# Performance work log

Hardware: AMD Instinct MI355X
Metric: run time of the kernel (lower is better)

Reference implementation:

```python
import jax, jax.numpy as jnp
import numpy as np

B, NT, NC, NN = 2, 64, 1024, 1024
C, H = 1024, 16
HD = C // H
N = NT + NC + NN
EPS = 1e-5
NEG = -1e30


def _ln(t, w, b):
    # LayerNorm over last dim (head_dim), torch eps=1e-5
    mu = jnp.mean(t, axis=-1, keepdims=True)
    var = jnp.mean(jnp.square(t - mu), axis=-1, keepdims=True)
    return (t - mu) * jax.lax.rsqrt(var + EPS) * w + b


def _rope(q, k, pos):
    # q,k: [B,H,S,HD]; pos: [B,S]; rotate-half RoPE, base 10000
    hd = q.shape[-1]
    half = hd // 2
    inv_freq = 1.0 / (10000.0 ** (jnp.arange(half, dtype=jnp.float32) / half))
    ang = pos.astype(jnp.float32)[:, None, :, None] * inv_freq  # [B,1,S,half]
    cos, sin = jnp.cos(ang), jnp.sin(ang)
    def rot(t):
        t1, t2 = t[..., :half], t[..., half:]
        return jnp.concatenate([t1 * cos - t2 * sin, t2 * cos + t1 * sin], axis=-1)
    return rot(q), rot(k)


def setup_inputs() -> dict:
    key = jax.random.key(0)
    ks = jax.random.split(key, 4)
    s = 0.02
    return {
        "x": jax.random.normal(ks[0], (B, N, C), jnp.float32),
        "position_ids": jnp.broadcast_to(jnp.arange(NC + NN, dtype=jnp.int32), (B, NC + NN)),
        "text_position_ids": jnp.broadcast_to(jnp.arange(NT, dtype=jnp.int32), (B, NT)),
        "attention_mask": jnp.tril(jnp.ones((N, N), dtype=bool)),
        "n_text": NT, "n_clean": NC, "n_noised": NN,
        "qkv_w": jax.random.normal(ks[1], (3, 3 * C, C), jnp.float32) * s,
        "qkv_b": jnp.zeros((3, 3 * C), jnp.float32),
        "qn_w": jnp.ones((3, HD), jnp.float32),
        "qn_b": jnp.zeros((3, HD), jnp.float32),
        "kn_w": jnp.ones((3, HD), jnp.float32),
        "kn_b": jnp.zeros((3, HD), jnp.float32),
        "proj_w": jax.random.normal(ks[2], (3, C, C), jnp.float32) * s,
        "proj_b": jnp.zeros((3, C), jnp.float32),
    }


def reference(x, position_ids, text_position_ids, attention_mask, n_text, n_clean, n_noised,
              qkv_w, qkv_b, qn_w, qn_b, kn_w, kn_b, proj_w, proj_b):
    Bx, Nx, Cx = x.shape
    hd = qn_w.shape[-1]
    nh = Cx // hd
    b0, b1 = n_text, n_text + n_clean
    segs = (x[:, :b0], x[:, b0:b1], x[:, b1:])  # text / clean / noised

    qs, kks, vvs = [], [], []
    for i, xs in enumerate(segs):
        S = xs.shape[1]
        qkv = jnp.einsum('bsc,oc->bso', xs, qkv_w[i]) + qkv_b[i]
        qkv = qkv.reshape(Bx, S, 3, nh, hd).transpose(2, 0, 3, 1, 4)  # [3,B,H,S,hd]
        q = _ln(qkv[0], qn_w[i], qn_b[i])
        k = _ln(qkv[1], kn_w[i], kn_b[i])
        qs.append(q); kks.append(k); vvs.append(qkv[2])

    img_q = jnp.concatenate([qs[1], qs[2]], axis=2)
    img_k = jnp.concatenate([kks[1], kks[2]], axis=2)
    img_q, img_k = _rope(img_q, img_k, position_ids)
    txt_q, txt_k = _rope(qs[0], kks[0], text_position_ids)

    q = jnp.concatenate([txt_q, img_q], axis=2)
    k = jnp.concatenate([txt_k, img_k], axis=2)
    v = jnp.concatenate(vvs, axis=2)

    scale = 1.0 / np.sqrt(hd).astype(np.float32)
    scores = jnp.einsum('bhqd,bhkd->bhqk', q, k) * scale
    scores = jnp.where(attention_mask, scores, NEG)
    attn = jax.nn.softmax(scores, axis=-1)
    out = jnp.einsum('bhqk,bhkd->bhqd', attn, v)
    out = out.transpose(0, 2, 1, 3).reshape(Bx, Nx, Cx)

    o_segs = (out[:, :b0], out[:, b0:b1], out[:, b1:])
    outs = [jnp.einsum('bsc,oc->bso', o_segs[i], proj_w[i]) + proj_b[i] for i in range(3)]
    return jnp.concatenate(outs, axis=1)
```

## Files before the change

kernel.cpp:

```cpp
#include <hip/hip_runtime.h>
#include <hip/hip_bf16.h>

#define BB   2
#define NT   64
#define NC   1024
#define NN   1024
#define NTOK (NT + NC + NN)
#define CC   1024
#define HH   16
#define HD   64
#define K3   (3 * CC)
#define EPSV 1e-5f

typedef __attribute__((ext_vector_type(8))) short short8;
typedef __attribute__((ext_vector_type(4))) float f32x4;
typedef __attribute__((ext_vector_type(4))) float float4v;

__device__ __forceinline__ short bf16raw(float x) {
    __hip_bfloat16 h = __float2bfloat16(x);
    return *(short*)&h;
}

#define GL_LDS(gptr, lptr) \
    __builtin_amdgcn_global_load_lds( \
        (const __attribute__((address_space(1))) void*)(gptr), \
        (__attribute__((address_space(3))) void*)(lptr), 16, 0, 0)

__global__ __launch_bounds__(256) void cast_all(
    const float* __restrict__ s0, const float* __restrict__ s1, const float* __restrict__ s2,
    __hip_bfloat16* __restrict__ d0, __hip_bfloat16* __restrict__ d1, __hip_bfloat16* __restrict__ d2,
    int n0, int n1, int n2)
{
    int i = blockIdx.x * 256 + threadIdx.x;
    int stride = gridDim.x * 256;
    int ntot = n0 + n1 + n2;
    for (; i < ntot; i += stride) {
        const float* sp; short* dp; int j;
        if (i < n0)            { sp = s0; dp = (short*)d0; j = i; }
        else if (i < n0 + n1)  { sp = s1; dp = (short*)d1; j = i - n0; }
        else                   { sp = s2; dp = (short*)d2; j = i - n0 - n1; }
        float4v v = *(const float4v*)(sp + (size_t)j * 4);
        short4 o;
        o.x = bf16raw(v.x); o.y = bf16raw(v.y); o.z = bf16raw(v.z); o.w = bf16raw(v.w);
        *(short4*)(dp + (size_t)j * 4) = o;
    }
}

__global__ __launch_bounds__(256) void gemm_qkv(
    const __hip_bfloat16* __restrict__ A,
    const __hip_bfloat16* __restrict__ Wb,
    const float* __restrict__ biasb,
    const int* __restrict__ pos_ids,
    const int* __restrict__ tpos_ids,
    const float* __restrict__ qn_w, const float* __restrict__ qn_b,
    const float* __restrict__ kn_w, const float* __restrict__ kn_b,
    __hip_bfloat16* __restrict__ Q,
    __hip_bfloat16* __restrict__ Kg,
    __hip_bfloat16* __restrict__ Vt)
{
    __shared__ short buf[128 * 134];
    short* As = buf;
    short* Bs = buf + 8192;

    int tid = threadIdx.x;
    int lane = tid & 63, w = tid >> 6;
    int l15 = lane & 15, quad = lane >> 4;
    int wm = w >> 1, wn = w & 1;
    int r7 = l15 & 7;

    int y = blockIdx.y;
    int seg, tm;
    if (y < 16)      { seg = 1; tm = y * 128; }
    else if (y < 32) { seg = 2; tm = (y - 16) * 128; }
    else             { seg = 0; tm = 0; }
    int S = (seg == 0) ? 64 : 1024;
    int seg_start = (seg == 0) ? 0 : (seg == 1 ? NT : NT + NC);
    const short* W = (const short*)Wb + (size_t)seg * K3 * CC;
    const float* bias = biasb + (size_t)seg * K3;
    int tileN = blockIdx.x * 128;

    const short* aptr[4];
    const short* bptr[4];
#pragma unroll
    for (int j = 0; j < 4; ++j) {
        int c = j * 256 + tid;
        int row = c >> 3, u = (c & 7) ^ (row & 7);
        int ar = tm + row;
        int arow = (ar / S) * NTOK + seg_start + (ar % S);
        aptr[j] = (const short*)A + (size_t)arow * CC + u * 8;
        bptr[j] = W + (size_t)(tileN + row) * CC + u * 8;
    }

    f32x4 zero = {0.f, 0.f, 0.f, 0.f};
    f32x4 acc[4][4];
#pragma unroll
    for (int mb = 0; mb < 4; ++mb)
#pragma unroll
        for (int nb = 0; nb < 4; ++nb) acc[mb][nb] = zero;

    for (int k0 = 0; k0 < CC; k0 += 64) {
        __syncthreads();
#pragma unroll
        for (int j = 0; j < 4; ++j) {
            int c8 = (j * 256 + tid) * 8;
            GL_LDS(aptr[j] + k0, As + c8);
            GL_LDS(bptr[j] + k0, Bs + c8);
        }
        __syncthreads();

#pragma unroll
        for (int s = 0; s < 2; ++s) {
            int sx = ((s * 4 + quad) ^ r7) * 8;
            short8 af[4], bf[4];
#pragma unroll
            for (int mb = 0; mb < 4; ++mb)
                af[mb] = *(const short8*)&As[(wm * 64 + mb * 16 + l15) * 64 + sx];
#pragma unroll
            for (int nb = 0; nb < 4; ++nb)
                bf[nb] = *(const short8*)&Bs[(wn * 64 + nb * 16 + l15) * 64 + sx];
#pragma unroll
            for (int mb = 0; mb < 4; ++mb)
#pragma unroll
                for (int nb = 0; nb < 4; ++nb)
                    acc[mb][nb] = __builtin_amdgcn_mfma_f32_16x16x32_bf16(af[mb], bf[nb], acc[mb][nb], 0, 0, 0);
        }
    }

    int sect = tileN >> 10;
    __syncthreads();

    if (sect < 2) {
        const float* nw = (sect == 0 ? qn_w : kn_w) + seg * HD;
        const float* nbv = (sect == 0 ? qn_b : kn_b) + seg * HD;
        float lw[4], lb[4], bcol[4];
#pragma unroll
        for (int nb = 0; nb < 4; ++nb) {
            lw[nb] = nw[nb * 16 + l15];
            lb[nb] = nbv[nb * 16 + l15];
            bcol[nb] = bias[tileN + wn * 64 + nb * 16 + l15];
        }
        float invf0 = expf(-9.210340371976184f * (float)l15 * (1.0f / 32.0f));
        float invf1 = expf(-9.210340371976184f * (float)(16 + l15) * (1.0f / 32.0f));
        float qscale = (sect == 0) ? 0.125f : 1.0f;

#pragma unroll
        for (int mb = 0; mb < 4; ++mb) {
#pragma unroll
            for (int r = 0; r < 4; ++r) {
                int tok = wm * 64 + mb * 16 + quad * 4 + r;
                int ar = tm + tok;
                int bb = ar / S;
                int nloc = seg_start + (ar % S);
                float v[4];
#pragma unroll
                for (int nb = 0; nb < 4; ++nb) v[nb] = acc[mb][nb][r] + bcol[nb];

                float mu = v[0] + v[1] + v[2] + v[3];
#pragma unroll
                for (int off = 8; off >= 1; off >>= 1) mu += __shfl_xor(mu, off);
                mu *= (1.0f / 64.0f);
                float t[4];
                float var = 0.f;
#pragma unroll
                for (int nb = 0; nb < 4; ++nb) { t[nb] = v[nb] - mu; var += t[nb] * t[nb]; }
#pragma unroll
                for (int off = 8; off >= 1; off >>= 1) var += __shfl_xor(var, off);
                var *= (1.0f / 64.0f);
                float rstd = rsqrtf(var + EPSV);
#pragma unroll
                for (int nb = 0; nb < 4; ++nb) v[nb] = t[nb] * rstd * lw[nb] + lb[nb];

                int pos = (seg == 0) ? tpos_ids[bb * NT + nloc]
                                     : pos_ids[bb * (NC + NN) + (nloc - NT)];
                float s0, c0, s1, c1;
                sincosf((float)pos * invf0, &s0, &c0);
                sincosf((float)pos * invf1, &s1, &c1);
                short* bp = &buf[tok * 134 + wn * 64];
                bp[0 * 16 + l15] = bf16raw((v[0] * c0 - v[2] * s0) * qscale);
                bp[1 * 16 + l15] = bf16raw((v[1] * c1 - v[3] * s1) * qscale);
                bp[2 * 16 + l15] = bf16raw((v[2] * c0 + v[0] * s0) * qscale);
                bp[3 * 16 + l15] = bf16raw((v[3] * c1 + v[1] * s1) * qscale);
            }
        }
        __syncthreads();
        __hip_bfloat16* dst = (sect == 0) ? Q : Kg;
        int head_base = (tileN & 1023) >> 6;
#pragma unroll
        for (int it = 0; it < 8; ++it) {
            int idx = it * 256 + tid;
            int tok = idx >> 4, cc = (idx & 15) * 8;
            int ar = tm + tok;
            int bb = ar / S;
            int nloc = seg_start + (ar % S);
            int hh2 = head_base + (cc >> 6), d = cc & 63;
            *(short8*)((short*)dst + ((size_t)(bb * HH + hh2) * NTOK + nloc) * HD + d) =
                *(const short8*)&buf[tok * 134 + cc];
        }
    } else {
        float bcol[4];
#pragma unroll
        for (int nb = 0; nb < 4; ++nb) bcol[nb] = bias[tileN + wn * 64 + nb * 16 + l15];
#pragma unroll
        for (int mb = 0; mb < 4; ++mb) {
#pragma unroll
            for (int r = 0; r < 4; ++r) {
                int tok = wm * 64 + mb * 16 + quad * 4 + r;
#pragma unroll
                for (int nb = 0; nb < 4; ++nb) {
                    int col = wn * 64 + nb * 16 + l15;
                    buf[col * 134 + tok] = bf16raw(acc[mb][nb][r] + bcol[nb]);
                }
            }
        }
        __syncthreads();
#pragma unroll
        for (int it = 0; it < 8; ++it) {
            int idx = it * 256 + tid;
            int row = idx >> 4;
            int tc = (idx & 15) * 8;
            int vcol = (tileN - 2048) + row;
            int h = vcol >> 6, d = vcol & 63;
            int ar = tm + tc;
            int bb = ar / S;
            int nloc = seg_start + (ar % S);
            short8 val = *(const short8*)&buf[row * 134 + tc];
            *(short8*)((short*)Vt + ((size_t)(bb * HH + h) * HD + d) * NTOK + nloc) = val;
        }
    }
}

__global__ __launch_bounds__(256) void gemm_proj(
    const __hip_bfloat16* __restrict__ A,
    const __hip_bfloat16* __restrict__ Wb,
    const float* __restrict__ biasb,
    float* __restrict__ Cout)
{
    __shared__ short As[64 * 64];
    __shared__ short Bs[128 * 64];

    int tid = threadIdx.x;
    int lane = tid & 63, w = tid >> 6;
    int l15 = lane & 15, quad = lane >> 4;
    int wm = w >> 1, wn = w & 1;
    int r7 = l15 & 7;

    int y = blockIdx.y;
    int seg, tm;
    if (y < 32)      { seg = 1; tm = y * 64; }
    else if (y < 64) { seg = 2; tm = (y - 32) * 64; }
    else             { seg = 0; tm = (y - 64) * 64; }
    int S = (seg == 0) ? 64 : 1024;
    int seg_start = (seg == 0) ? 0 : (seg == 1 ? NT : NT + NC);
    const short* W = (const short*)Wb + (size_t)seg * CC * CC;
    const float* bias = biasb + (size_t)seg * CC;
    int tileN = blockIdx.x * 128;

    const short* aptr[2];
    const short* bptr[4];
#pragma unroll
    for (int j = 0; j < 2; ++j) {
        int c = j * 256 + tid;
        int row = c >> 3, u = (c & 7) ^ (row & 7);
        int ar = tm + row;
        int arow = (ar / S) * NTOK + seg_start + (ar % S);
        aptr[j] = (const short*)A + (size_t)arow * CC + u * 8;
    }
#pragma unroll
    for (int j = 0; j < 4; ++j) {
        int c = j * 256 + tid;
        int row = c >> 3, u = (c & 7) ^ (row & 7);
        bptr[j] = W + (size_t)(tileN + row) * CC + u * 8;
    }

    f32x4 zero = {0.f, 0.f, 0.f, 0.f};
    f32x4 acc[2][4];
#pragma unroll
    for (int mb = 0; mb < 2; ++mb)
#pragma unroll
        for (int nb = 0; nb < 4; ++nb) acc[mb][nb] = zero;

    for (int k0 = 0; k0 < CC; k0 += 64) {
        __syncthreads();
#pragma unroll
        for (int j = 0; j < 2; ++j)
            GL_LDS(aptr[j] + k0, As + (j * 256 + tid) * 8);
#pragma unroll
        for (int j = 0; j < 4; ++j)
            GL_LDS(bptr[j] + k0, Bs + (j * 256 + tid) * 8);
        __syncthreads();

#pragma unroll
        for (int s = 0; s < 2; ++s) {
            int sx = ((s * 4 + quad) ^ r7) * 8;
            short8 af[2], bf[4];
#pragma unroll
            for (int mb = 0; mb < 2; ++mb)
                af[mb] = *(const short8*)&As[(wm * 32 + mb * 16 + l15) * 64 + sx];
#pragma unroll
            for (int nb = 0; nb < 4; ++nb)
                bf[nb] = *(const short8*)&Bs[(wn * 64 + nb * 16 + l15) * 64 + sx];
#pragma unroll
            for (int mb = 0; mb < 2; ++mb)
#pragma unroll
                for (int nb = 0; nb < 4; ++nb)
                    acc[mb][nb] = __builtin_amdgcn_mfma_f32_16x16x32_bf16(af[mb], bf[nb], acc[mb][nb], 0, 0, 0);
        }
    }

#pragma unroll
    for (int mb = 0; mb < 2; ++mb) {
#pragma unroll
        for (int r = 0; r < 4; ++r) {
            int ar = tm + wm * 32 + mb * 16 + quad * 4 + r;
            int crow = (ar / S) * NTOK + seg_start + (ar % S);
            float* cp = Cout + (size_t)crow * CC + tileN;
#pragma unroll
            for (int nb = 0; nb < 4; ++nb) {
                int col = wn * 64 + nb * 16 + l15;
                cp[col] = acc[mb][nb][r] + bias[tileN + col];
            }
        }
    }
}

__global__ __launch_bounds__(256) void attn_mfma(
    const __hip_bfloat16* __restrict__ Q,
    const __hip_bfloat16* __restrict__ Kg,
    const __hip_bfloat16* __restrict__ Vt,
    __hip_bfloat16* __restrict__ O)
{
    __shared__ short Ks[128][72];
    __shared__ short Vs[64][136];
    __shared__ short Ps[4][16][136];

    int tid = threadIdx.x;
    int lane = tid & 63, w = tid >> 6;
    int quad = lane >> 4, l15 = lane & 15;
    int bh = blockIdx.y, b = bh >> 4, h = bh & 15;
    int q0 = (gridDim.x - 1 - blockIdx.x) * 64;
    size_t base = (size_t)bh * NTOK * HD;

    int qrow = q0 + w * 16 + l15;
    short8 qf0 = *(const short8*)((const short*)Q + base + (size_t)qrow * HD + quad * 8);
    short8 qf1 = *(const short8*)((const short*)Q + base + (size_t)qrow * HD + 32 + quad * 8);

    f32x4 zero = {0.f, 0.f, 0.f, 0.f};
    f32x4 oacc[4] = {zero, zero, zero, zero};
    float l[4] = {0.f, 0.f, 0.f, 0.f};

    int qmax_w = q0 + w * 16 + 15;
    int ntiles = (q0 + 191) >> 7;

    for (int t = 0; t < ntiles; ++t) {
        __syncthreads();
        for (int i = tid; i < 2048; i += 256) {
            if (i < 1024) {
                int kr = i >> 3, kc = (i & 7) * 8;
                int row = t * 128 + kr;
                if (row >= NTOK) row = NTOK - 1;
                *(short8*)&Ks[kr][kc] = *(const short8*)((const short*)Kg + base + (size_t)row * HD + kc);
            } else {
                int j = i - 1024;
                int vr = j >> 4, vc = (j & 15) * 8;
                int col = t * 128 + vc;
                if (col + 8 > NTOK) col = NTOK - 8;
                *(short8*)&Vs[vr][vc] = *(const short8*)((const short*)Vt + base + (size_t)vr * NTOK + col);
            }
        }
        __syncthreads();
        if (t * 128 > qmax_w) continue;

#pragma unroll
        for (int half = 0; half < 2; ++half) {
            f32x4 s[4];
#pragma unroll
            for (int kb4 = 0; kb4 < 4; ++kb4) {
                int kb = half * 4 + kb4;
                short8 kf0 = *(const short8*)&Ks[kb * 16 + l15][quad * 8];
                short8 kf1 = *(const short8*)&Ks[kb * 16 + l15][32 + quad * 8];
                f32x4 z = zero;
                z = __builtin_amdgcn_mfma_f32_16x16x32_bf16(qf0, kf0, z, 0, 0, 0);
                z = __builtin_amdgcn_mfma_f32_16x16x32_bf16(qf1, kf1, z, 0, 0, 0);
                s[kb4] = z;
            }
#pragma unroll
            for (int r = 0; r < 4; ++r) {
                int qg = q0 + w * 16 + quad * 4 + r;
#pragma unroll
                for (int kb4 = 0; kb4 < 4; ++kb4) {
                    int kgk = t * 128 + (half * 4 + kb4) * 16 + l15;
                    float p = (kgk <= qg) ? __expf(s[kb4][r]) : 0.f;
                    Ps[w][quad * 4 + r][(half * 4 + kb4) * 16 + l15] = bf16raw(p);
                    l[r] += p;
                }
            }
        }

        __builtin_amdgcn_wave_barrier();

#pragma unroll
        for (int sl = 0; sl < 4; ++sl) {
            short8 pf = *(const short8*)&Ps[w][l15][sl * 32 + quad * 8];
#pragma unroll
            for (int db = 0; db < 4; ++db) {
                short8 vf = *(const short8*)&Vs[db * 16 + l15][sl * 32 + quad * 8];
                oacc[db] = __builtin_amdgcn_mfma_f32_16x16x32_bf16(pf, vf, oacc[db], 0, 0, 0);
            }
        }
    }

#pragma unroll
    for (int r = 0; r < 4; ++r) {
#pragma unroll
        for (int off = 8; off >= 1; off >>= 1) l[r] += __shfl_xor(l[r], off);
    }

#pragma unroll
    for (int r = 0; r < 4; ++r) {
        int qg = q0 + w * 16 + quad * 4 + r;
        float inv_l = 1.0f / l[r];
#pragma unroll
        for (int db = 0; db < 4; ++db) {
            O[(size_t)(b * NTOK + qg) * CC + h * HD + db * 16 + l15] =
                __float2bfloat16(oacc[db][r] * inv_l);
        }
    }
}

extern "C" void kernel_launch(void* const* d_in, const int* in_sizes, int n_in,
                              void* d_out, int out_size, void* d_ws, size_t ws_size,
                              hipStream_t stream) {
    const float* x      = (const float*)d_in[0];
    const int* pos_ids  = (const int*)d_in[1];
    const int* tpos_ids = (const int*)d_in[2];
    const float* qkv_w  = (const float*)d_in[7];
    const float* qkv_b  = (const float*)d_in[8];
    const float* qn_w   = (const float*)d_in[9];
    const float* qn_b   = (const float*)d_in[10];
    const float* kn_w   = (const float*)d_in[11];
    const float* kn_b   = (const float*)d_in[12];
    const float* proj_w = (const float*)d_in[13];
    const float* proj_b = (const float*)d_in[14];
    float* out = (float*)d_out;

    const size_t n_x    = (size_t)BB * NTOK * CC;
    const size_t n_qkvw = (size_t)3 * K3 * CC;
    const size_t n_prjw = (size_t)3 * CC * CC;

    __hip_bfloat16* x_bf    = (__hip_bfloat16*)d_ws;
    __hip_bfloat16* qkvw_bf = x_bf + n_x;
    __hip_bfloat16* prjw_bf = qkvw_bf + n_qkvw;
    __hip_bfloat16* Qbf  = prjw_bf + n_prjw;
    __hip_bfloat16* Kbf  = Qbf + n_x;
    __hip_bfloat16* Vtbf = Kbf + n_x;
    __hip_bfloat16* attn_bf = x_bf;

    cast_all<<<1024, 256, 0, stream>>>(x, qkv_w, proj_w, x_bf, qkvw_bf, prjw_bf,
                                       (int)(n_x / 4), (int)(n_qkvw / 4), (int)(n_prjw / 4));

    gemm_qkv<<<dim3(K3 / 128, 33), 256, 0, stream>>>(
        x_bf, qkvw_bf, qkv_b, pos_ids, tpos_ids,
        qn_w, qn_b, kn_w, kn_b, Qbf, Kbf, Vtbf);

    attn_mfma<<<dim3(NTOK / 64, BB * HH), 256, 0, stream>>>(Qbf, Kbf, Vtbf, attn_bf);

    gemm_proj<<<dim3(CC / 128, 66), 256, 0, stream>>>(attn_bf, prjw_bf, proj_b, out);
}
```

Measured before the change: 320.9 us.

## Restructure attention to 128-query blocks with swizzled LDS and direct global-to-LDS loads

The attention kernel now uses 512-thread blocks covering 128 queries (8 waves) and 64-key tiles instead of 256 threads, 64 queries and 128-key tiles. K and V tiles are loaded straight into LDS with global_load_lds, using an XOR swizzle in place of padded rows to avoid bank conflicts. This halves the number of K/V loads per query and drops the register round-trip on staging. In exchange there are more loop iterations, each with two block-wide barriers, and bounds clamping for the final partial query block.

```diff
diff --git a/kernel.cpp b/kernel.cpp
--- a/kernel.cpp
+++ b/kernel.cpp
@@ -323,87 +323,86 @@
     }
 }
 
-__global__ __launch_bounds__(256) void attn_mfma(
+__global__ __launch_bounds__(512) void attn_mfma(
     const __hip_bfloat16* __restrict__ Q,
     const __hip_bfloat16* __restrict__ Kg,
     const __hip_bfloat16* __restrict__ Vt,
     __hip_bfloat16* __restrict__ O)
 {
-    __shared__ short Ks[128][72];
-    __shared__ short Vs[64][136];
-    __shared__ short Ps[4][16][136];
+    __shared__ short Ks[64 * 64];
+    __shared__ short Vs[64 * 64];
+    __shared__ short Ps[8][16 * 72];
 
     int tid = threadIdx.x;
     int lane = tid & 63, w = tid >> 6;
     int quad = lane >> 4, l15 = lane & 15;
+    int r7 = l15 & 7;
     int bh = blockIdx.y, b = bh >> 4, h = bh & 15;
-    int q0 = (gridDim.x - 1 - blockIdx.x) * 64;
+    int q0 = (gridDim.x - 1 - blockIdx.x) * 128;
     size_t base = (size_t)bh * NTOK * HD;
 
     int qrow = q0 + w * 16 + l15;
-    short8 qf0 = *(const short8*)((const short*)Q + base + (size_t)qrow * HD + quad * 8);
-    short8 qf1 = *(const short8*)((const short*)Q + base + (size_t)qrow * HD + 32 + quad * 8);
+    int qr_c = qrow < NTOK ? qrow : NTOK - 1;
+    short8 qf0 = *(const short8*)((const short*)Q + base + (size_t)qr_c * HD + quad * 8);
+    short8 qf1 = *(const short8*)((const short*)Q + base + (size_t)qr_c * HD + 32 + quad * 8);
+
+    int srow = tid >> 3;
+    int su = (tid & 7) ^ (srow & 7);
+    const short* kptr = (const short*)Kg + base + (size_t)srow * HD + su * 8;
+    const short* vptr = (const short*)Vt + base + (size_t)srow * NTOK + su * 8;
+    int c8 = tid * 8;
 
     f32x4 zero = {0.f, 0.f, 0.f, 0.f};
     f32x4 oacc[4] = {zero, zero, zero, zero};
     float l[4] = {0.f, 0.f, 0.f, 0.f};
 
     int qmax_w = q0 + w * 16 + 15;
-    int ntiles = (q0 + 191) >> 7;
+    int nt_cov = q0 / 64 + 2;
+    int ntiles = nt_cov < 33 ? nt_cov : 33;
+
+    int sx0 = (quad ^ r7) * 8;
+    int sx1 = ((4 + quad) ^ r7) * 8;
 
     for (int t = 0; t < ntiles; ++t) {
         __syncthreads();
-        for (int i = tid; i < 2048; i += 256) {
-            if (i < 1024) {
-                int kr = i >> 3, kc = (i & 7) * 8;
-                int row = t * 128 + kr;
-                if (row >= NTOK) row = NTOK - 1;
-                *(short8*)&Ks[kr][kc] = *(const short8*)((const short*)Kg + base + (size_t)row * HD + kc);
-            } else {
-                int j = i - 1024;
-                int vr = j >> 4, vc = (j & 15) * 8;
-                int col = t * 128 + vc;
-                if (col + 8 > NTOK) col = NTOK - 8;
-                *(short8*)&Vs[vr][vc] = *(const short8*)((const short*)Vt + base + (size_t)vr * NTOK + col);
+        GL_LDS(kptr + (size_t)(t * 64) * HD, Ks + c8);
+        GL_LDS(vptr + t * 64, Vs + c8);
+        __syncthreads();
+        if (t * 64 > qmax_w) continue;
+
+        f32x4 s[4];
+#pragma unroll
+        for (int kb = 0; kb < 4; ++kb) {
+            int krow = (kb * 16 + l15) * 64;
+            short8 kf0 = *(const short8*)&Ks[krow + sx0];
+            short8 kf1 = *(const short8*)&Ks[krow + sx1];
+            f32x4 z = zero;
+            z = __builtin_amdgcn_mfma_f32_16x16x32_bf16(qf0, kf0, z, 0, 0, 0);
+            z = __builtin_amdgcn_mfma_f32_16x16x32_bf16(qf1, kf1, z, 0, 0, 0);
+            s[kb] = z;
+        }
+
+#pragma unroll
+        for (int r = 0; r < 4; ++r) {
+            int qg = q0 + w * 16 + quad * 4 + r;
+#pragma unroll
+            for (int kb = 0; kb < 4; ++kb) {
+                int kgk = t * 64 + kb * 16 + l15;
+                float p = (kgk <= qg) ? __expf(s[kb][r]) : 0.f;
+                Ps[w][(quad * 4 + r) * 72 + kb * 16 + l15] = bf16raw(p);
+                l[r] += p;
             }
         }
-        __syncthreads();
-        if (t * 128 > qmax_w) continue;
-
-#pragma unroll
-        for (int half = 0; half < 2; ++half) {
-            f32x4 s[4];
-#pragma unroll
-            for (int kb4 = 0; kb4 < 4; ++kb4) {
-                int kb = half * 4 + kb4;
-                short8 kf0 = *(const short8*)&Ks[kb * 16 + l15][quad * 8];
-                short8 kf1 = *(const short8*)&Ks[kb * 16 + l15][32 + quad * 8];
-                f32x4 z = zero;
-                z = __builtin_amdgcn_mfma_f32_16x16x32_bf16(qf0, kf0, z, 0, 0, 0);
-                z = __builtin_amdgcn_mfma_f32_16x16x32_bf16(qf1, kf1, z, 0, 0, 0);
-                s[kb4] = z;
-            }
-#pragma unroll
-            for (int r = 0; r < 4; ++r) {
-                int qg = q0 + w * 16 + quad * 4 + r;
-#pragma unroll
-                for (int kb4 = 0; kb4 < 4; ++kb4) {
-                    int kgk = t * 128 + (half * 4 + kb4) * 16 + l15;
-                    float p = (kgk <= qg) ? __expf(s[kb4][r]) : 0.f;
-                    Ps[w][quad * 4 + r][(half * 4 + kb4) * 16 + l15] = bf16raw(p);
-                    l[r] += p;
-                }
-            }
-        }
 
         __builtin_amdgcn_wave_barrier();
 
 #pragma unroll
-        for (int sl = 0; sl < 4; ++sl) {
-            short8 pf = *(const short8*)&Ps[w][l15][sl * 32 + quad * 8];
+        for (int sl = 0; sl < 2; ++sl) {
+            short8 pf = *(const short8*)&Ps[w][l15 * 72 + sl * 32 + quad * 8];
+            int vsx = ((sl * 4 + quad) ^ r7) * 8;
 #pragma unroll
             for (int db = 0; db < 4; ++db) {
-                short8 vf = *(const short8*)&Vs[db * 16 + l15][sl * 32 + quad * 8];
+                short8 vf = *(const short8*)&Vs[(db * 16 + l15) * 64 + vsx];
                 oacc[db] = __builtin_amdgcn_mfma_f32_16x16x32_bf16(pf, vf, oacc[db], 0, 0, 0);
             }
         }
@@ -418,6 +417,7 @@
 #pragma unroll
     for (int r = 0; r < 4; ++r) {
         int qg = q0 + w * 16 + quad * 4 + r;
+        if (qg >= NTOK) continue;
         float inv_l = 1.0f / l[r];
 #pragma unroll
         for (int db = 0; db < 4; ++db) {
@@ -462,7 +462,7 @@
         x_bf, qkvw_bf, qkv_b, pos_ids, tpos_ids,
         qn_w, qn_b, kn_w, kn_b, Qbf, Kbf, Vtbf);
 
-    attn_mfma<<<dim3(NTOK / 64, BB * HH), 256, 0, stream>>>(Qbf, Kbf, Vtbf, attn_bf);
+    attn_mfma<<<dim3((NTOK + 127) / 128, BB * HH), 512, 0, stream>>>(Qbf, Kbf, Vtbf, attn_bf);
 
     gemm_proj<<<dim3(CC / 128, 66), 256, 0, stream>>>(attn_bf, prjw_bf, proj_b, out);
 }
```

Result: faster. 293.0 us (-8.7%).
